# Kernel optimization log

Measured on AMD Instinct MI355X. Metric: run time of the kernel, lower is better.

The kernel has to match this reference:

```python
import jax, jax.numpy as jnp
import numpy as np

B, H, W, CP, CI = 2, 256, 256, 256, 256
IN, OUT = CP + CI, CP          # in_dims=512, out_dims=256
WS, NH, L = 8, 8, 2            # window, heads, num blocks
N = WS * WS                    # tokens per window
HD = OUT // NH                 # head dim = 32
SCALE = HD ** -0.5

def _rel_pos_index():
    c = np.stack(np.meshgrid(np.arange(WS), np.arange(WS), indexing='ij')).reshape(2, -1)
    r = (c[:, :, None] - c[:, None, :]).transpose(1, 2, 0)
    r[..., 0] += WS - 1
    r[..., 1] += WS - 1
    r[..., 0] *= 2 * WS - 1
    return r.sum(-1)  # [N, N] int

REL_IDX = _rel_pos_index()

def _attn_mask(shift):
    img = np.zeros((H, W))
    cnt = 0
    for hs in (slice(0, -WS), slice(-WS, -shift), slice(-shift, None)):
        for ws_ in (slice(0, -WS), slice(-WS, -shift), slice(-shift, None)):
            img[hs, ws_] = cnt
            cnt += 1
    m = img.reshape(H // WS, WS, W // WS, WS).transpose(0, 2, 1, 3).reshape(-1, N)
    d = m[:, None, :] - m[:, :, None]
    return jnp.asarray(np.where(d != 0, -100.0, 0.0).astype(np.float32))  # [nW, N, N]

MASK = _attn_mask(WS // 2)

def _ln(x, g, b, eps=1e-5):
    m = x.mean(-1, keepdims=True)
    v = ((x - m) ** 2).mean(-1, keepdims=True)
    return (x - m) * jax.lax.rsqrt(v + eps) * g + b

def _win_attn(x, qkv_w, qkv_b, rpb_t, proj_w, proj_b, shift):
    # x: [B,H,W,C]
    if shift > 0:
        x = jnp.roll(x, (-shift, -shift), axis=(1, 2))
    nW = (H // WS) * (W // WS)
    xw = x.reshape(B, H // WS, WS, W // WS, WS, OUT).transpose(0, 1, 3, 2, 4, 5).reshape(B, nW, N, OUT)
    qkv = (xw @ qkv_w.T + qkv_b).reshape(B, nW, N, 3, NH, HD)
    q, k, v = qkv[..., 0, :, :], qkv[..., 1, :, :], qkv[..., 2, :, :]  # [B,nW,N,NH,HD]
    attn = jnp.einsum('bwqhd,bwkhd->bwhqk', q * SCALE, k)  # [B,nW,NH,N,N]
    bias = rpb_t[REL_IDX.reshape(-1)].reshape(N, N, NH).transpose(2, 0, 1)  # [NH,N,N]
    attn = attn + bias
    if shift > 0:
        attn = attn + MASK[None, :, None, :, :]
    attn = jax.nn.softmax(attn, axis=-1)
    out = jnp.einsum('bwhqk,bwkhd->bwqhd', attn, v).reshape(B, nW, N, OUT)
    out = out @ proj_w.T + proj_b
    out = out.reshape(B, H // WS, W // WS, WS, WS, OUT).transpose(0, 1, 3, 2, 4, 5).reshape(B, H, W, OUT)
    if shift > 0:
        out = jnp.roll(out, (shift, shift), axis=(1, 2))
    return out

def setup_inputs() -> dict:
    key = jax.random.key(0)
    ks = jax.random.split(key, 12)
    s = 0.02
    p = {}
    p['pcd'] = jax.random.normal(ks[0], (B, H, W, CP), jnp.float32)
    p['img'] = jax.random.normal(ks[1], (B, H, W, CI), jnp.float32)
    p['rd_w1'] = jax.random.normal(ks[2], (4 * IN, IN), jnp.float32) * s
    p['rd_b1'] = jnp.zeros((4 * IN,), jnp.float32)
    p['rd_lng'] = jnp.ones((4 * IN,), jnp.float32)
    p['rd_lnb'] = jnp.zeros((4 * IN,), jnp.float32)
    p['rd_w2'] = jax.random.normal(ks[3], (OUT, 4 * IN), jnp.float32) * s
    p['rd_b2'] = jnp.zeros((OUT,), jnp.float32)
    p['n1g'] = jnp.ones((L, OUT), jnp.float32)
    p['n1b'] = jnp.zeros((L, OUT), jnp.float32)
    p['qkv_w'] = jax.random.normal(ks[4], (L, 3 * OUT, OUT), jnp.float32) * s
    p['qkv_b'] = jnp.zeros((L, 3 * OUT), jnp.float32)
    p['rpb'] = jax.random.normal(ks[5], (L, (2 * WS - 1) ** 2, NH), jnp.float32) * s
    p['proj_w'] = jax.random.normal(ks[6], (L, OUT, OUT), jnp.float32) * s
    p['proj_b'] = jnp.zeros((L, OUT), jnp.float32)
    p['n2g'] = jnp.ones((L, OUT), jnp.float32)
    p['n2b'] = jnp.zeros((L, OUT), jnp.float32)
    p['mlp_w1'] = jax.random.normal(ks[7], (L, 4 * OUT, OUT), jnp.float32) * s
    p['mlp_b1'] = jnp.zeros((L, 4 * OUT), jnp.float32)
    p['mlp_w2'] = jax.random.normal(ks[8], (L, OUT, 4 * OUT), jnp.float32) * s
    p['mlp_b2'] = jnp.zeros((L, OUT), jnp.float32)
    return p

def reference(pcd, img, rd_w1, rd_b1, rd_lng, rd_lnb, rd_w2, rd_b2,
              n1g, n1b, qkv_w, qkv_b, rpb, proj_w, proj_b,
              n2g, n2b, mlp_w1, mlp_b1, mlp_w2, mlp_b2):
    # reduce_dim: Linear -> LeakyReLU(0.01) -> LayerNorm -> Linear
    x = jnp.concatenate([pcd, img], axis=3)
    x = x @ rd_w1.T + rd_b1
    x = jnp.where(x > 0, x, 0.01 * x)
    x = _ln(x, rd_lng, rd_lnb)
    x = x @ rd_w2.T + rd_b2
    # two SwinTransformerBlocks (shift 0, then WS//2)
    for i in range(L):
        shift = 0 if i % 2 == 0 else WS // 2
        x = x + _win_attn(_ln(x, n1g[i], n1b[i]), qkv_w[i], qkv_b[i], rpb[i], proj_w[i], proj_b[i], shift)
        h = _ln(x, n2g[i], n2b[i])
        h = jax.nn.gelu(h @ mlp_w1[i].T + mlp_b1[i], approximate=False)
        x = x + h @ mlp_w2[i].T + mlp_b2[i]
    return x + pcd
```

## Files before the change

kernel.cpp:

```cpp
#include <hip/hip_runtime.h>
#include <math.h>

typedef __attribute__((ext_vector_type(4))) float f32x4v;
typedef __attribute__((ext_vector_type(8))) __bf16 bf16x8v;
typedef __attribute__((ext_vector_type(2))) uint u32x2v;
typedef __attribute__((ext_vector_type(4))) uint u32x4v;

#define SCALE 0.17677669529663687f
#define TOK 131072
#define MCHUNK 32768
#define T32 ((long)TOK * 32)
#define C32 ((long)MCHUNK * 32)

__device__ __forceinline__ ushort f2bf(float v){
  uint x = __float_as_uint(v);
  return (ushort)((x + 0x7fffu + ((x >> 16) & 1u)) >> 16);
}
__device__ __forceinline__ float bflo(uint u){ return __uint_as_float(u << 16); }
__device__ __forceinline__ float bfhi(uint u){ return __uint_as_float(u & 0xffff0000u); }
__device__ __forceinline__ float bf2f(ushort u){ return __uint_as_float((uint)u << 16); }

__global__ __launch_bounds__(256) void cvtw_k(const float* __restrict__ src,
    ushort* __restrict__ dst, int K, long m32, int n4){
  const int i = blockIdx.x * 256 + threadIdx.x;
  if (i >= n4) return;
  const int flat = i * 4;
  const int r = flat / K, k = flat % K;
  float4 v = ((const float4*)src)[i];
  ushort4 o = { f2bf(v.x), f2bf(v.y), f2bf(v.z), f2bf(v.w) };
  *(ushort4*)(dst + (long)(k >> 5) * m32 + (long)r * 32 + (k & 31)) = o;
}

__global__ __launch_bounds__(64) void cvtwg_k(const float* __restrict__ src,
    const float* __restrict__ gma, const float* __restrict__ bta,
    ushort* __restrict__ dst, float* __restrict__ c1, float* __restrict__ c2,
    int K, long m32){
  const int n = blockIdx.x, lane = threadIdx.x;
  const float* sp = src + (long)n * K;
  float s1 = 0.f, s2 = 0.f;
  for (int k = lane * 4; k < K; k += 256){
    float4 wv = *(const float4*)(sp + k);
    float4 gv = *(const float4*)(gma + k);
    float4 bv = *(const float4*)(bta + k);
    s1 += wv.x * gv.x + wv.y * gv.y + wv.z * gv.z + wv.w * gv.w;
    s2 += wv.x * bv.x + wv.y * bv.y + wv.z * bv.z + wv.w * bv.w;
    ushort4 o = { f2bf(wv.x * gv.x), f2bf(wv.y * gv.y), f2bf(wv.z * gv.z), f2bf(wv.w * gv.w) };
    *(ushort4*)(dst + (long)(k >> 5) * m32 + (long)n * 32 + (k & 31)) = o;
  }
  #pragma unroll
  for (int o = 1; o < 64; o <<= 1){ s1 += __shfl_xor(s1, o); s2 += __shfl_xor(s2, o); }
  if (lane == 0){ c1[n] = s1; c2[n] = s2; }
}

__global__ __launch_bounds__(256) void concat_k(const float* __restrict__ pcd,
    const float* __restrict__ img, ushort* __restrict__ A0){
  const long gid = (long)blockIdx.x * 256 + threadIdx.x;
  const long t = gid >> 7;
  const int c4 = (int)(gid & 127) * 4;
  const float* src = (c4 < 256) ? (pcd + t * 256 + c4) : (img + t * 256 + (c4 - 256));
  float4 v = *(const float4*)src;
  ushort4 o = { f2bf(v.x), f2bf(v.y), f2bf(v.z), f2bf(v.w) };
  const long chunk = t >> 15, tc = t & 32767;
  ushort* dst = A0 + chunk * 16777216 + (long)(c4 >> 5) * C32 + tc * 32 + (c4 & 31);
  __builtin_nontemporal_store(*(u32x2v*)&o, (u32x2v*)dst);
}

__global__ __launch_bounds__(256) void rowstats_k(const ushort* __restrict__ X,
    float* __restrict__ stats){
  const int row = blockIdx.x, tid = threadIdx.x;
  uint4 u = *(const uint4*)(X + (long)(tid >> 2) * C32 + (long)row * 32 + (tid & 3) * 8);
  float s = 0.f, q = 0.f;
  uint* e = (uint*)&u;
  #pragma unroll
  for (int c = 0; c < 4; ++c){
    float a = bflo(e[c]), b2 = bfhi(e[c]);
    s += a + b2; q += a * a + b2 * b2;
  }
  #pragma unroll
  for (int o = 1; o < 64; o <<= 1){ s += __shfl_xor(s, o); q += __shfl_xor(q, o); }
  __shared__ float ss[4], qs[4];
  if ((tid & 63) == 0){ ss[tid >> 6] = s; qs[tid >> 6] = q; }
  __syncthreads();
  if (tid == 0){
    float S = ss[0] + ss[1] + ss[2] + ss[3];
    float Q = qs[0] + qs[1] + qs[2] + qs[3];
    float mean = S * (1.f / 2048.f);
    float var = Q * (1.f / 2048.f) - mean * mean;
    stats[row * 2] = mean;
    stats[row * 2 + 1] = rsqrtf(var + 1e-5f);
  }
}

__global__ __launch_bounds__(256) void stats256b_k(const ushort* __restrict__ xb,
    float* __restrict__ stats){
  const int lane = threadIdx.x & 63, wd = threadIdx.x >> 6;
  const long row = (long)blockIdx.x * 4 + wd;
  uint2 u = *(const uint2*)(xb + (long)(lane >> 3) * T32 + row * 32 + (lane & 7) * 4);
  float a = bflo(u.x), b2 = bfhi(u.x), c = bflo(u.y), d = bfhi(u.y);
  float s = a + b2 + c + d;
  float q = a * a + b2 * b2 + c * c + d * d;
  #pragma unroll
  for (int o = 1; o < 64; o <<= 1){ s += __shfl_xor(s, o); q += __shfl_xor(q, o); }
  if (lane == 0){
    float mean = s * (1.f / 256.f);
    float var = q * (1.f / 256.f) - mean * mean;
    stats[row * 2] = mean;
    stats[row * 2 + 1] = rsqrtf(var + 1e-5f);
  }
}

template<int ACT, int OUTT, int RES, bool LNEPI, int MINB>
__global__ __launch_bounds__(256, MINB) void gemm_k(
    const ushort* __restrict__ A, const ushort* __restrict__ W,
    const float* __restrict__ bias,
    float* __restrict__ outf, ushort* __restrict__ outb,
    const ushort* __restrict__ res, const float* __restrict__ pcdp,
    const float* __restrict__ stats, const float* __restrict__ c1v,
    const float* __restrict__ c2v, int N, int K, int gx,
    long aM32, long wM32, long oM32, int mOff)
{
  __shared__ ushort SH[16384];
  const int tid = threadIdx.x;
  const int lane = tid & 63, w = tid >> 6;
  const int nwg = gridDim.x;
  const int xcd = blockIdx.x & 7;
  const int idx = blockIdx.x >> 3;
  const int mPerX = nwg / (8 * gx);
  const int sg = idx / (8 * gx);
  const int u  = idx - sg * (8 * gx);
  const int nT = u >> 3;
  const int ml = u & 7;
  const int mBase = (xcd * mPerX + sg * 8 + ml) * 128;
  const int nBase = nT * 128;
  const int fr = lane & 15, grp = lane >> 4;
  const int wr = w >> 1, wc = w & 1;

  f32x4v acc[4][4];
  #pragma unroll
  for (int i = 0; i < 4; ++i)
    #pragma unroll
    for (int j = 0; j < 4; ++j) acc[i][j] = (f32x4v){0.f, 0.f, 0.f, 0.f};

  const long aBase = (long)(mBase + w * 32) * 32 + lane * 8;
  const long wBase = (long)(nBase + w * 32) * 32 + lane * 8;
  ushort* Ad0 = &SH[w * 1024 + lane * 8];
  ushort* Bd0 = &SH[4096 + w * 1024 + lane * 8];
  ushort* Ad1 = &SH[8192 + w * 1024 + lane * 8];
  ushort* Bd1 = &SH[12288 + w * 1024 + lane * 8];

  const int NT = K >> 5;

#define MFMASTEP(ao, bo) do { \
    bf16x8v af[4], bv[4]; \
    _Pragma("unroll") \
    for (int i = 0; i < 4; ++i) \
      af[i] = *(const bf16x8v*)&SH[(ao) + (wr * 64 + i * 16 + fr) * 32 + grp * 8]; \
    _Pragma("unroll") \
    for (int j = 0; j < 4; ++j) \
      bv[j] = *(const bf16x8v*)&SH[(bo) + (wc * 64 + j * 16 + fr) * 32 + grp * 8]; \
    _Pragma("unroll") \
    for (int i = 0; i < 4; ++i) \
      _Pragma("unroll") \
      for (int j = 0; j < 4; ++j) \
        acc[i][j] = __builtin_amdgcn_mfma_f32_16x16x32_bf16(af[i], bv[j], acc[i][j], 0, 0, 0); \
  } while (0)

  {
    uint4 x0 = *(const uint4*)(A + aBase);
    uint4 x1 = *(const uint4*)(A + aBase + 512);
    uint4 y0 = *(const uint4*)(W + wBase);
    uint4 y1 = *(const uint4*)(W + wBase + 512);
    *(uint4*)Ad0 = x0; *(uint4*)(Ad0 + 512) = x1;
    *(uint4*)Bd0 = y0; *(uint4*)(Bd0 + 512) = y1;
  }
  uint4 pa0 = *(const uint4*)(A + aBase + aM32);
  uint4 pa1 = *(const uint4*)(A + aBase + aM32 + 512);
  uint4 pb0 = *(const uint4*)(W + wBase + wM32);
  uint4 pb1 = *(const uint4*)(W + wBase + wM32 + 512);
  uint4 qa0 = *(const uint4*)(A + aBase + 2 * aM32);
  uint4 qa1 = *(const uint4*)(A + aBase + 2 * aM32 + 512);
  uint4 qb0 = *(const uint4*)(W + wBase + 2 * wM32);
  uint4 qb1 = *(const uint4*)(W + wBase + 2 * wM32 + 512);
  __syncthreads();

  for (int t = 0; t < NT; t += 2){
    MFMASTEP(0, 4096);
    *(uint4*)Ad1 = pa0; *(uint4*)(Ad1 + 512) = pa1;
    *(uint4*)Bd1 = pb0; *(uint4*)(Bd1 + 512) = pb1;
    if (t + 3 < NT){
      const long ao = aBase + (long)(t + 3) * aM32;
      const long wo = wBase + (long)(t + 3) * wM32;
      pa0 = *(const uint4*)(A + ao);
      pa1 = *(const uint4*)(A + ao + 512);
      pb0 = *(const uint4*)(W + wo);
      pb1 = *(const uint4*)(W + wo + 512);
    }
    __syncthreads();
    MFMASTEP(8192, 12288);
    if (t + 2 < NT){
      *(uint4*)Ad0 = qa0; *(uint4*)(Ad0 + 512) = qa1;
      *(uint4*)Bd0 = qb0; *(uint4*)(Bd0 + 512) = qb1;
      if (t + 4 < NT){
        const long ao = aBase + (long)(t + 4) * aM32;
        const long wo = wBase + (long)(t + 4) * wM32;
        qa0 = *(const uint4*)(A + ao);
        qa1 = *(const uint4*)(A + ao + 512);
        qb0 = *(const uint4*)(W + wo);
        qb1 = *(const uint4*)(W + wo + 512);
      }
    }
    __syncthreads();
  }
#undef MFMASTEP

  float muv[16], rsv[16];
  if (LNEPI){
    #pragma unroll
    for (int i = 0; i < 4; ++i)
      #pragma unroll
      for (int rr = 0; rr < 4; ++rr){
        const int m = mBase + wr * 64 + i * 16 + grp * 4 + rr;
        muv[i * 4 + rr] = stats[m * 2];
        rsv[i * 4 + rr] = stats[m * 2 + 1];
      }
  }
  #pragma unroll
  for (int j = 0; j < 4; ++j){
    const int n = nBase + wc * 64 + j * 16 + fr;
    const float bn = bias[n];
    float c1n = 0.f, c2n = 0.f;
    if (LNEPI){ c1n = c1v[n]; c2n = c2v[n]; }
    #pragma unroll
    for (int i = 0; i < 4; ++i){
      #pragma unroll
      for (int rr = 0; rr < 4; ++rr){
        const long m = mBase + wr * 64 + i * 16 + grp * 4 + rr;
        float v = acc[i][j][rr];
        if (LNEPI) v = rsv[i * 4 + rr] * v - muv[i * 4 + rr] * rsv[i * 4 + rr] * c1n + c2n;
        v += bn;
        if (ACT == 1) v = v > 0.f ? v : 0.01f * v;
        if (ACT == 2){
          const float u2 = v * (0.7978845608f + 0.0356774081f * v * v);
          const float t2 = 1.f - 2.f / (__expf(2.f * u2) + 1.f);
          v = 0.5f * v * (1.f + t2);
        }
        if (RES >= 1)
          v += bf2f(res[(long)(n >> 5) * T32 + (mOff + m) * 32 + (n & 31)]);
        if (RES == 2) v += pcdp[(mOff + m) * N + n];
        acc[i][j][rr] = v;
        if (OUTT == 0) __builtin_nontemporal_store(v, &outf[(mOff + m) * N + n]);
      }
    }
  }
  if (OUTT == 1){
    ushort* eb = &SH[0];
    __syncthreads();
    #pragma unroll
    for (int p = 0; p < 2; ++p){
      if (wr == p){
        #pragma unroll
        for (int i = 0; i < 4; ++i)
          #pragma unroll
          for (int rr = 0; rr < 4; ++rr){
            const int rl = i * 16 + grp * 4 + rr;
            #pragma unroll
            for (int j = 0; j < 4; ++j)
              eb[rl * 128 + wc * 64 + j * 16 + fr] = f2bf(acc[i][j][rr]);
          }
      }
      __syncthreads();
      #pragma unroll
      for (int it = 0; it < 4; ++it){
        const int c = it * 256 + tid;
        const int row = c >> 4, cg = c & 15;
        const u32x4v val = *(const u32x4v*)&eb[row * 128 + cg * 8];
        ushort* dst = outb + (long)((nBase >> 5) + (cg >> 2)) * oM32
                    + (long)(mOff + mBase + p * 64 + row) * 32 + (cg & 3) * 8;
        __builtin_nontemporal_store(val, (u32x4v*)dst);
      }
      __syncthreads();
    }
  }
}

template<int SHIFT>
__global__ __launch_bounds__(256, 2) void attn_k(const ushort* __restrict__ qkv,
    const float* __restrict__ rpb, ushort* __restrict__ outp)
{
  __shared__ ushort Vt[4][2312];
  __shared__ ushort Pl[4][4616];
  __shared__ float bias_s[4][226];
  __shared__ int code_s[64];
  const int tid = threadIdx.x;
  const int lane = tid & 63, wid = tid >> 6;
  const int hg = blockIdx.x & 1;
  const int bw = blockIdx.x >> 1;
  const int b = bw >> 10, widx = bw & 1023;
  const int wh = widx >> 5, ww = widx & 31;
  const int head = hg * 4 + wid;
  const int fr = lane & 15, grp = lane >> 4;

  for (int i = lane; i < 225; i += 64) bias_s[wid][i] = rpb[i * 8 + head];
  if (SHIFT > 0 && tid < 64){
    const int hh = wh * 8 + (tid >> 3), wwp = ww * 8 + (tid & 7);
    const int rh = (hh < 248) ? 0 : ((hh < 256 - SHIFT) ? 1 : 2);
    const int rw = (wwp < 248) ? 0 : ((wwp < 256 - SHIFT) ? 1 : 2);
    code_s[tid] = rh * 3 + rw;
  }
  #pragma unroll
  for (int it = 0; it < 4; ++it){
    const int c = it * 256 + tid;
    const int row = c >> 4, part = c & 15;
    const int hc = part >> 2, dc = part & 3;
    const int hs = (wh * 8 + (row >> 3) + SHIFT) & 255;
    const int wsm = (ww * 8 + (row & 7) + SHIFT) & 255;
    const long tk = ((long)b * 256 + hs) * 256 + wsm;
    const uint4 vu = *(const uint4*)(qkv + (long)(16 + hg * 4 + hc) * T32 + tk * 32 + dc * 8);
    const ushort* ve = (const ushort*)&vu;
    #pragma unroll
    for (int e = 0; e < 8; ++e)
      Vt[hc][(dc * 8 + e) * 72 + row] = ve[e];
  }
  long tokr[4];
  #pragma unroll
  for (int j = 0; j < 4; ++j){
    const int n = j * 16 + fr;
    const int hs = (wh * 8 + (n >> 3) + SHIFT) & 255;
    const int wsm = (ww * 8 + (n & 7) + SHIFT) & 255;
    tokr[j] = ((long)b * 256 + hs) * 256 + wsm;
  }
  bf16x8v kf[4];
  #pragma unroll
  for (int j = 0; j < 4; ++j)
    kf[j] = *(const bf16x8v*)(qkv + (long)(8 + head) * T32 + tokr[j] * 32 + grp * 8);
  __syncthreads();

  float invs[4][4];
  #pragma unroll
  for (int qi = 0; qi < 4; ++qi){
    const bf16x8v qf = *(const bf16x8v*)(qkv + (long)head * T32 + tokr[qi] * 32 + grp * 8);
    f32x4v sc[4];
    #pragma unroll
    for (int ci = 0; ci < 4; ++ci)
      sc[ci] = __builtin_amdgcn_mfma_f32_16x16x32_bf16(qf, kf[ci],
          (f32x4v){0.f, 0.f, 0.f, 0.f}, 0, 0, 0);
    #pragma unroll
    for (int rr = 0; rr < 4; ++rr){
      const int q = qi * 16 + grp * 4 + rr;
      const int thq = q >> 3, twq = q & 7;
      int codeq = 0;
      if (SHIFT > 0){
        const int hq = wh * 8 + thq, wq = ww * 8 + twq;
        const int rh = (hq < 248) ? 0 : ((hq < 256 - SHIFT) ? 1 : 2);
        const int rw = (wq < 248) ? 0 : ((wq < 256 - SHIFT) ? 1 : 2);
        codeq = rh * 3 + rw;
      }
      const int lbase = (thq + 7 - (fr >> 3)) * 15 + (twq + 7 - (fr & 7));
      float sum = 0.f;
      #pragma unroll
      for (int ci = 0; ci < 4; ++ci){
        float s = sc[ci][rr] * SCALE + bias_s[wid][lbase - ci * 30];
        if (SHIFT > 0 && codeq != code_s[ci * 16 + fr]) s -= 100.f;
        const float p = __expf(s);
        sum += p;
        Pl[wid][q * 72 + ci * 16 + fr] = f2bf(p);
      }
      sum += __shfl_xor(sum, 1);
      sum += __shfl_xor(sum, 2);
      sum += __shfl_xor(sum, 4);
      sum += __shfl_xor(sum, 8);
      invs[qi][rr] = 1.f / sum;
    }
  }
  f32x4v o[4][2];
  #pragma unroll
  for (int qi = 0; qi < 4; ++qi)
    #pragma unroll
    for (int di = 0; di < 2; ++di) o[qi][di] = (f32x4v){0.f, 0.f, 0.f, 0.f};
  #pragma unroll
  for (int ks = 0; ks < 2; ++ks){
    bf16x8v pa[4], bvv[2];
    #pragma unroll
    for (int qi = 0; qi < 4; ++qi)
      pa[qi] = *(const bf16x8v*)&Pl[wid][(qi * 16 + fr) * 72 + ks * 32 + grp * 8];
    #pragma unroll
    for (int di = 0; di < 2; ++di)
      bvv[di] = *(const bf16x8v*)&Vt[wid][(di * 16 + fr) * 72 + ks * 32 + grp * 8];
    #pragma unroll
    for (int qi = 0; qi < 4; ++qi)
      #pragma unroll
      for (int di = 0; di < 2; ++di)
        o[qi][di] = __builtin_amdgcn_mfma_f32_16x16x32_bf16(pa[qi], bvv[di], o[qi][di], 0, 0, 0);
  }
  #pragma unroll
  for (int qi = 0; qi < 4; ++qi)
    #pragma unroll
    for (int di = 0; di < 2; ++di)
      #pragma unroll
      for (int rr = 0; rr < 4; ++rr)
        Pl[wid][(qi * 16 + grp * 4 + rr) * 72 + di * 16 + fr] =
            f2bf(o[qi][di][rr] * invs[qi][rr]);
  {
    const int n = lane;
    const int hs = (wh * 8 + (n >> 3) + SHIFT) & 255;
    const int wsm = (ww * 8 + (n & 7) + SHIFT) & 255;
    const long tokL = ((long)b * 256 + hs) * 256 + wsm;
    ushort* ob = outp + (long)head * T32 + tokL * 32;
    #pragma unroll
    for (int c4 = 0; c4 < 4; ++c4)
      *(uint4*)(ob + c4 * 8) = *(const uint4*)&Pl[wid][n * 72 + c4 * 8];
  }
}

extern "C" void kernel_launch(void* const* d_in, const int* in_sizes, int n_in,
                              void* d_out, int out_size, void* d_ws, size_t ws_size,
                              hipStream_t stream){
  const float* pcd    = (const float*)d_in[0];
  const float* img    = (const float*)d_in[1];
  const float* rd_w1  = (const float*)d_in[2];
  const float* rd_b1  = (const float*)d_in[3];
  const float* rd_lng = (const float*)d_in[4];
  const float* rd_lnb = (const float*)d_in[5];
  const float* rd_w2  = (const float*)d_in[6];
  const float* rd_b2  = (const float*)d_in[7];
  const float* n1g    = (const float*)d_in[8];
  const float* n1b    = (const float*)d_in[9];
  const float* qkv_w  = (const float*)d_in[10];
  const float* qkv_b  = (const float*)d_in[11];
  const float* rpb    = (const float*)d_in[12];
  const float* proj_w = (const float*)d_in[13];
  const float* proj_b = (const float*)d_in[14];
  const float* n2g    = (const float*)d_in[15];
  const float* n2b    = (const float*)d_in[16];
  const float* mlp_w1 = (const float*)d_in[17];
  const float* mlp_b1 = (const float*)d_in[18];
  const float* mlp_w2 = (const float*)d_in[19];
  const float* mlp_b2 = (const float*)d_in[20];

  char* ws = (char*)d_ws;
  ushort* w1b    = (ushort*)(ws + 0);
  ushort* w2g    = (ushort*)(ws + 2097152);
  ushort* qkvwg  = (ushort*)(ws + 3145728);
  ushort* projwb = (ushort*)(ws + 3932160);
  ushort* mlp1wg = (ushort*)(ws + 4194304);
  ushort* mlp2wb = (ushort*)(ws + 5242880);
  float*  cvec   = (float*)(ws + 6291456);
  float*  w2c1   = cvec,        *w2c2   = cvec + 256;
  float*  qkvc1  = cvec + 512,  *qkvc2  = cvec + 2048;
  float*  mlp1c1 = cvec + 3584, *mlp1c2 = cvec + 5632;
  float*  stats  = (float*)(ws + 6324224);
  ushort* xr     = (ushort*)(ws + 7372800);
  char*   big    = ws + 74481664;
  ushort* A0     = (ushort*)big;
  ushort* X1c    = (ushort*)(big + 134217728);
  ushort* qkvb   = (ushort*)big;
  ushort* attno  = (ushort*)(big + 201326592);
  ushort* hidden = (ushort*)big;
  float* xout = (float*)d_out;

  cvtw_k<<<1024, 256, 0, stream>>>(rd_w1, w1b, 512, 65536, 262144);
  cvtwg_k<<<256, 64, 0, stream>>>(rd_w2, rd_lng, rd_lnb, w2g, w2c1, w2c2, 2048, 8192);
  for (int i = 0; i < 2; ++i){
    cvtw_k<<<64,  256, 0, stream>>>(proj_w + i * 65536, projwb + i * 65536, 256, 8192, 16384);
    cvtw_k<<<256, 256, 0, stream>>>(mlp_w2 + i * 262144, mlp2wb + i * 262144, 1024, 8192, 65536);
    cvtwg_k<<<768, 64, 0, stream>>>(qkv_w + i * 196608, n1g + i * 256, n1b + i * 256,
        qkvwg + i * 196608, qkvc1 + i * 768, qkvc2 + i * 768, 256, 24576);
    cvtwg_k<<<1024, 64, 0, stream>>>(mlp_w1 + i * 262144, n2g + i * 256, n2b + i * 256,
        mlp1wg + i * 262144, mlp1c1 + i * 1024, mlp1c2 + i * 1024, 256, 32768);
  }
  concat_k<<<65536, 256, 0, stream>>>(pcd, img, A0);

  for (int c = 0; c < 4; ++c){
    const long off = (long)c * MCHUNK;
    gemm_k<1,1,0,false,2><<<4096, 256, 0, stream>>>(A0 + (long)c * 16777216, w1b, rd_b1,
        nullptr, X1c, nullptr, nullptr, nullptr, nullptr, nullptr,
        2048, 512, 16, C32, 65536, C32, 0);
    rowstats_k<<<MCHUNK, 256, 0, stream>>>(X1c, stats + off * 2);
    gemm_k<0,1,0,true,2><<<512, 256, 0, stream>>>(X1c, w2g, rd_b2,
        nullptr, xr, nullptr, nullptr,
        stats + off * 2, w2c1, w2c2,
        256, 2048, 2, C32, 8192, T32, (int)off);
  }
  stats256b_k<<<TOK / 4, 256, 0, stream>>>(xr, stats);

  for (int i = 0; i < 2; ++i){
    gemm_k<0,1,0,true,2><<<6144, 256, 0, stream>>>(xr, qkvwg + i * 196608, qkv_b + i * 768,
        nullptr, qkvb, nullptr, nullptr, stats, qkvc1 + i * 768, qkvc2 + i * 768,
        768, 256, 6, T32, 24576, T32, 0);
    if (i == 0)
      attn_k<0><<<4096, 256, 0, stream>>>(qkvb, rpb, attno);
    else
      attn_k<4><<<4096, 256, 0, stream>>>(qkvb, rpb + 1800, attno);
    gemm_k<0,1,1,false,2><<<2048, 256, 0, stream>>>(attno, projwb + i * 65536,
        proj_b + i * 256, nullptr, xr, xr, nullptr, nullptr, nullptr, nullptr,
        256, 256, 2, T32, 8192, T32, 0);
    stats256b_k<<<TOK / 4, 256, 0, stream>>>(xr, stats);
    gemm_k<2,1,0,true,2><<<8192, 256, 0, stream>>>(xr, mlp1wg + i * 262144,
        mlp_b1 + i * 1024, nullptr, hidden, nullptr, nullptr,
        stats, mlp1c1 + i * 1024, mlp1c2 + i * 1024,
        1024, 256, 8, T32, 32768, T32, 0);
    if (i == 0){
      gemm_k<0,1,1,false,2><<<2048, 256, 0, stream>>>(hidden, mlp2wb, mlp_b2,
          nullptr, xr, xr, nullptr, nullptr, nullptr, nullptr,
          256, 1024, 2, T32, 8192, T32, 0);
      stats256b_k<<<TOK / 4, 256, 0, stream>>>(xr, stats);
    } else {
      gemm_k<0,0,2,false,2><<<2048, 256, 0, stream>>>(hidden, mlp2wb + 262144,
          mlp_b2 + 256, xout, nullptr, xr, pcd, nullptr, nullptr, nullptr,
          256, 1024, 2, T32, 8192, T32, 0);
    }
  }
}
```

Measured before the change: 1.844 ms.

## Fuse LayerNorm row statistics into first reduce-dim GEMM epilogue

The first reduce-dim GEMM now accumulates per-row sums and sums of squares over its 128-column tile in the epilogue and writes them as partials into the output buffer, used as scratch. A tiny kernel then reduces the 64 partials per row into mean and rstd. This replaces the separate pass that re-read the full 2048-wide bf16 activation chunk. The catch is extra epilogue registers and shuffles, plus a runtime branch compiled into every GEMM instantiation. The stats now come from fp32 values before bf16 rounding.

```diff
diff --git a/kernel.cpp b/kernel.cpp
--- a/kernel.cpp
+++ b/kernel.cpp
@@ -65,30 +65,17 @@
   __builtin_nontemporal_store(*(u32x2v*)&o, (u32x2v*)dst);
 }
 
-__global__ __launch_bounds__(256) void rowstats_k(const ushort* __restrict__ X,
+__global__ __launch_bounds__(256) void statsred_k(const float* __restrict__ pb,
     float* __restrict__ stats){
-  const int row = blockIdx.x, tid = threadIdx.x;
-  uint4 u = *(const uint4*)(X + (long)(tid >> 2) * C32 + (long)row * 32 + (tid & 3) * 8);
+  const int row = blockIdx.x * 256 + threadIdx.x;
+  const float2* p = (const float2*)(pb + (long)row * 64);
   float s = 0.f, q = 0.f;
-  uint* e = (uint*)&u;
-  #pragma unroll
-  for (int c = 0; c < 4; ++c){
-    float a = bflo(e[c]), b2 = bfhi(e[c]);
-    s += a + b2; q += a * a + b2 * b2;
-  }
-  #pragma unroll
-  for (int o = 1; o < 64; o <<= 1){ s += __shfl_xor(s, o); q += __shfl_xor(q, o); }
-  __shared__ float ss[4], qs[4];
-  if ((tid & 63) == 0){ ss[tid >> 6] = s; qs[tid >> 6] = q; }
-  __syncthreads();
-  if (tid == 0){
-    float S = ss[0] + ss[1] + ss[2] + ss[3];
-    float Q = qs[0] + qs[1] + qs[2] + qs[3];
-    float mean = S * (1.f / 2048.f);
-    float var = Q * (1.f / 2048.f) - mean * mean;
-    stats[row * 2] = mean;
-    stats[row * 2 + 1] = rsqrtf(var + 1e-5f);
-  }
+  #pragma unroll
+  for (int i = 0; i < 32; ++i){ const float2 v = p[i]; s += v.x; q += v.y; }
+  const float mean = s * (1.f / 2048.f);
+  const float var = q * (1.f / 2048.f) - mean * mean;
+  stats[row * 2] = mean;
+  stats[row * 2 + 1] = rsqrtf(var + 1e-5f);
 }
 
 __global__ __launch_bounds__(256) void stats256b_k(const ushort* __restrict__ xb,
@@ -117,7 +104,7 @@
     const ushort* __restrict__ res, const float* __restrict__ pcdp,
     const float* __restrict__ stats, const float* __restrict__ c1v,
     const float* __restrict__ c2v, int N, int K, int gx,
-    long aM32, long wM32, long oM32, int mOff)
+    long aM32, long wM32, long oM32, int mOff, float* __restrict__ ost)
 {
   __shared__ ushort SH[16384];
   const int tid = threadIdx.x;
@@ -224,6 +211,11 @@
         rsv[i * 4 + rr] = stats[m * 2 + 1];
       }
   }
+  float rsum[16], rsq[16];
+  if (ost){
+    #pragma unroll
+    for (int t2 = 0; t2 < 16; ++t2){ rsum[t2] = 0.f; rsq[t2] = 0.f; }
+  }
   #pragma unroll
   for (int j = 0; j < 4; ++j){
     const int n = nBase + wc * 64 + j * 16 + fr;
@@ -248,7 +240,22 @@
           v += bf2f(res[(long)(n >> 5) * T32 + (mOff + m) * 32 + (n & 31)]);
         if (RES == 2) v += pcdp[(mOff + m) * N + n];
         acc[i][j][rr] = v;
+        if (ost){ rsum[i * 4 + rr] += v; rsq[i * 4 + rr] += v * v; }
         if (OUTT == 0) __builtin_nontemporal_store(v, &outf[(mOff + m) * N + n]);
+      }
+    }
+  }
+  if (ost){
+    const int nT4 = nT * 4 + wc * 2;
+    #pragma unroll
+    for (int t2 = 0; t2 < 16; ++t2){
+      float s = rsum[t2], q = rsq[t2];
+      #pragma unroll
+      for (int o = 1; o < 16; o <<= 1){ s += __shfl_xor(s, o); q += __shfl_xor(q, o); }
+      if (fr == 0){
+        const long m = mBase + wr * 64 + (t2 >> 2) * 16 + grp * 4 + (t2 & 3);
+        ost[m * 64 + nT4]     = s;
+        ost[m * 64 + nT4 + 1] = q;
       }
     }
   }
@@ -457,6 +464,7 @@
   ushort* attno  = (ushort*)(big + 201326592);
   ushort* hidden = (ushort*)big;
   float* xout = (float*)d_out;
+  float* pstat = (float*)d_out;
 
   cvtw_k<<<1024, 256, 0, stream>>>(rd_w1, w1b, 512, 65536, 262144);
   cvtwg_k<<<256, 64, 0, stream>>>(rd_w2, rd_lng, rd_lnb, w2g, w2c1, w2c2, 2048, 8192);
@@ -474,40 +482,40 @@
     const long off = (long)c * MCHUNK;
     gemm_k<1,1,0,false,2><<<4096, 256, 0, stream>>>(A0 + (long)c * 16777216, w1b, rd_b1,
         nullptr, X1c, nullptr, nullptr, nullptr, nullptr, nullptr,
-        2048, 512, 16, C32, 65536, C32, 0);
-    rowstats_k<<<MCHUNK, 256, 0, stream>>>(X1c, stats + off * 2);
+        2048, 512, 16, C32, 65536, C32, 0, pstat);
+    statsred_k<<<128, 256, 0, stream>>>(pstat, stats + off * 2);
     gemm_k<0,1,0,true,2><<<512, 256, 0, stream>>>(X1c, w2g, rd_b2,
         nullptr, xr, nullptr, nullptr,
         stats + off * 2, w2c1, w2c2,
-        256, 2048, 2, C32, 8192, T32, (int)off);
+        256, 2048, 2, C32, 8192, T32, (int)off, nullptr);
   }
   stats256b_k<<<TOK / 4, 256, 0, stream>>>(xr, stats);
 
   for (int i = 0; i < 2; ++i){
     gemm_k<0,1,0,true,2><<<6144, 256, 0, stream>>>(xr, qkvwg + i * 196608, qkv_b + i * 768,
         nullptr, qkvb, nullptr, nullptr, stats, qkvc1 + i * 768, qkvc2 + i * 768,
-        768, 256, 6, T32, 24576, T32, 0);
+        768, 256, 6, T32, 24576, T32, 0, nullptr);
     if (i == 0)
       attn_k<0><<<4096, 256, 0, stream>>>(qkvb, rpb, attno);
     else
       attn_k<4><<<4096, 256, 0, stream>>>(qkvb, rpb + 1800, attno);
     gemm_k<0,1,1,false,2><<<2048, 256, 0, stream>>>(attno, projwb + i * 65536,
         proj_b + i * 256, nullptr, xr, xr, nullptr, nullptr, nullptr, nullptr,
-        256, 256, 2, T32, 8192, T32, 0);
+        256, 256, 2, T32, 8192, T32, 0, nullptr);
     stats256b_k<<<TOK / 4, 256, 0, stream>>>(xr, stats);
     gemm_k<2,1,0,true,2><<<8192, 256, 0, stream>>>(xr, mlp1wg + i * 262144,
         mlp_b1 + i * 1024, nullptr, hidden, nullptr, nullptr,
         stats, mlp1c1 + i * 1024, mlp1c2 + i * 1024,
-        1024, 256, 8, T32, 32768, T32, 0);
+        1024, 256, 8, T32, 32768, T32, 0, nullptr);
     if (i == 0){
       gemm_k<0,1,1,false,2><<<2048, 256, 0, stream>>>(hidden, mlp2wb, mlp_b2,
           nullptr, xr, xr, nullptr, nullptr, nullptr, nullptr,
-          256, 1024, 2, T32, 8192, T32, 0);
+          256, 1024, 2, T32, 8192, T32, 0, nullptr);
       stats256b_k<<<TOK / 4, 256, 0, stream>>>(xr, stats);
     } else {
       gemm_k<0,0,2,false,2><<<2048, 256, 0, stream>>>(hidden, mlp2wb + 262144,
           mlp_b2 + 256, xout, nullptr, xr, pcd, nullptr, nullptr, nullptr,
-          256, 1024, 2, T32, 8192, T32, 0);
-    }
-  }
-}
+          256, 1024, 2, T32, 8192, T32, 0, nullptr);
+    }
+  }
+}
```

Result: no change. 1.812 ms (-1.7%).
